# Kernel tuning notes

Hardware: AMD Instinct MI355X
Metric: run time of the kernel (lower is better)

## Reference

```python
import jax, jax.numpy as jnp
import numpy as np

E = 512        # embed_dim
H = 16         # num_heads
R = 8          # num_relation_heads
NH = H - R     # num_normal_heads
HD = E // H    # head_dim
SCALING = HD ** -0.5
B, LQ, LK = 2, 2048, 2048


def setup_inputs() -> dict:
    key = jax.random.key(0)
    ks = jax.random.split(key, 14)
    s = 1.0 / np.sqrt(E)  # keep pre-softmax logits moderate so exp() is stable
    inp = {
        "query": jax.random.normal(ks[0], (B, LQ, E), jnp.float32),
        "key": jax.random.normal(ks[1], (B, LK, E), jnp.float32),
        "value": jax.random.normal(ks[2], (B, LK, E), jnp.float32),
        "relation_weights": jax.random.uniform(ks[3], (B, R, LQ, LK), jnp.float32),
        "Wq": jax.random.normal(ks[4], (E, E), jnp.float32) * s,
        "bq": jnp.zeros((E,), jnp.float32),
        "Wk": jax.random.normal(ks[5], (E, E), jnp.float32) * s,
        "bk": jnp.zeros((E,), jnp.float32),
        "Wv": jax.random.normal(ks[6], (E, E), jnp.float32) * s,
        "bv": jnp.zeros((E,), jnp.float32),
        "Wo": jax.random.normal(ks[7], (E, E), jnp.float32) * s,
        "bo": jnp.zeros((E,), jnp.float32),
        "ln_gamma": jnp.ones((E,), jnp.float32),
        "ln_beta": jnp.zeros((E,), jnp.float32),
    }
    return inp


def reference(query, key, value, relation_weights, Wq, bq, Wk, bk, Wv, bv, Wo, bo, ln_gamma, ln_beta):
    b, lq, _ = query.shape
    lk = key.shape[1]
    # projections; weights stored as [in, out] so y = x @ W + b
    q = (query @ Wq + bq).reshape(b, lq, H, HD)
    k = (key @ Wk + bk).reshape(b, lk, H, HD)
    v = (value @ Wv + bv).reshape(b, lk, H, HD)
    # scores: [B, H, Lq, Lk]
    scores = jnp.einsum("bqhd,bkhd->bhqk", q, k) * SCALING
    # normal heads: standard softmax
    normal_attn = jax.nn.softmax(scores[:, :NH], axis=-1)
    # relation heads: exp(scores) * relation_weights, renormalized
    rel = jnp.exp(scores[:, NH:]) * relation_weights
    rel = rel / (rel.sum(axis=-1, keepdims=True) + 1e-6)
    attn = jnp.concatenate([normal_attn, rel], axis=1)  # [B, H, Lq, Lk]
    # weighted values -> [B, Lq, E]
    out = jnp.einsum("bhqk,bkhd->bqhd", attn, v).reshape(b, lq, E)
    out = out @ Wo + bo
    # LayerNorm (eps=1e-5, torch default)
    mu = out.mean(axis=-1, keepdims=True)
    var = out.var(axis=-1, keepdims=True)
    out = (out - mu) * jax.lax.rsqrt(var + 1e-5) * ln_gamma + ln_beta
    return out
```

## Files before the change

### kernel.cpp

```cpp
#include <hip/hip_runtime.h>


using u16 = unsigned short;
using u32 = unsigned int;

typedef __attribute__((ext_vector_type(8))) short bf16x8;
typedef __attribute__((ext_vector_type(4))) float f32x4;

#define H_  16
#define NH_ 8
#define HD_ 32
#define L_  2048
#define E_  512
#define B_  2
#define M_  4096
#define KSPLIT 2
static constexpr float SCALE_ = 0.1767766952966369f;

__device__ inline u16 f2bf(float x) {
  union { float f; u32 u; } v; v.f = x;
  u32 r = v.u + 0x7FFFu + ((v.u >> 16) & 1u);
  return (u16)(r >> 16);
}
__device__ inline u16 f2h(float x) {
  union { _Float16 h; u16 u; } v; v.h = (_Float16)x; return v.u;
}
__device__ inline float h2f(u16 x) {
  union { u16 u; _Float16 h; } v; v.u = x; return (float)v.h;
}

__global__ __launch_bounds__(256) void k_cvt3(const float* __restrict__ a, const float* __restrict__ b,
                                              const float* __restrict__ c,
                                              u16* __restrict__ oa, u16* __restrict__ ob, u16* __restrict__ oc) {
  int w = blockIdx.y;
  const float* s = (w == 0) ? a : (w == 1) ? b : c;
  u16* d = (w == 0) ? oa : (w == 1) ? ob : oc;
  size_t i = ((size_t)blockIdx.x * 256 + threadIdx.x) * 4;
  float4 v = *(const float4*)(s + i);
  uint2 pk;
  pk.x = (u32)f2bf(v.x) | ((u32)f2bf(v.y) << 16);
  pk.y = (u32)f2bf(v.z) | ((u32)f2bf(v.w) << 16);
  *(uint2*)(d + i) = pk;
}

__global__ __launch_bounds__(256) void k_wtrans(const float* __restrict__ Wq, const float* __restrict__ Wk,
                                                const float* __restrict__ Wv, const float* __restrict__ Wo,
                                                u16* __restrict__ Tq, u16* __restrict__ Tk,
                                                u16* __restrict__ Tv, u16* __restrict__ To) {
  int z = blockIdx.z;
  const float* W = (z == 0) ? Wq : (z == 1) ? Wk : (z == 2) ? Wv : Wo;
  u16* T = (z == 0) ? Tq : (z == 1) ? Tk : (z == 2) ? Tv : To;
  __shared__ u16 tile[64][65];
  int r0 = blockIdx.y * 64, c0 = blockIdx.x * 64;
  int tw = threadIdx.x >> 6, tl = threadIdx.x & 63;
#pragma unroll
  for (int i = 0; i < 16; ++i) {
    int r = i * 4 + tw;
    tile[r][tl] = f2bf(W[(size_t)(r0 + r) * E_ + c0 + tl]);
  }
  __syncthreads();
#pragma unroll
  for (int i = 0; i < 16; ++i) {
    int r = i * 4 + tw;
    T[(size_t)(c0 + r) * E_ + r0 + tl] = tile[tl][r];
  }
}

template <int MODE>
__device__ inline void gemm_body(const u16* __restrict__ A, const u16* __restrict__ Bt,
                                 const float* __restrict__ bias, void* __restrict__ out) {
  __shared__ __align__(16) u16 smem[2 * 128 * 72];
  u16* As = smem;
  u16* Bs = smem + 128 * 72;
  const int tid = threadIdx.x;
  const int lane = tid & 63, wid = tid >> 6;
  const int m0 = blockIdx.x * 128, n0 = blockIdx.y * 128;
  const int wm = (wid >> 1) * 64, wn = (wid & 1) * 64;
  const int mrow = lane & 15, quad = lane >> 4;
  f32x4 acc[4][4] = {};
  for (int k0 = 0; k0 < 512; k0 += 64) {
    __syncthreads();
#pragma unroll
    for (int i = 0; i < 4; ++i) {
      int task = i * 256 + tid;
      int r = task >> 3, c = task & 7;
      *(uint4*)(As + r * 72 + c * 8) = *(const uint4*)(A + (size_t)(m0 + r) * 512 + k0 + c * 8);
      *(uint4*)(Bs + r * 72 + c * 8) = *(const uint4*)(Bt + (size_t)(n0 + r) * 512 + k0 + c * 8);
    }
    __syncthreads();
#pragma unroll
    for (int kk = 0; kk < 64; kk += 32) {
      bf16x8 af[4], bfr[4];
#pragma unroll
      for (int f = 0; f < 4; ++f)
        af[f] = *(const bf16x8*)(As + (wm + f * 16 + mrow) * 72 + kk + quad * 8);
#pragma unroll
      for (int f = 0; f < 4; ++f)
        bfr[f] = *(const bf16x8*)(Bs + (wn + f * 16 + mrow) * 72 + kk + quad * 8);
#pragma unroll
      for (int fm = 0; fm < 4; ++fm)
#pragma unroll
        for (int fn = 0; fn < 4; ++fn)
          acc[fm][fn] = __builtin_amdgcn_mfma_f32_16x16x32_bf16(af[fm], bfr[fn], acc[fm][fn], 0, 0, 0);
    }
  }
  if (MODE == 0) {
    __syncthreads();
    u16* wscr = smem + wid * (64 * 72);
#pragma unroll
    for (int fn = 0; fn < 4; ++fn) {
      float bv = bias[n0 + wn + fn * 16 + mrow];
#pragma unroll
      for (int fm = 0; fm < 4; ++fm)
#pragma unroll
        for (int r = 0; r < 4; ++r)
          wscr[(fm * 16 + quad * 4 + r) * 72 + fn * 16 + mrow] = f2bf(acc[fm][fn][r] + bv);
    }
    asm volatile("s_waitcnt lgkmcnt(0)" ::: "memory");
    const int hg0 = (n0 + wn) >> 5;
#pragma unroll
    for (int c = 0; c < 8; ++c) {
      int linear = c * 64 + lane;
      int hh = linear >> 8;
      int rem = linear & 255;
      int lm = rem >> 2, j = rem & 3;
      uint4 vv = *(const uint4*)(wscr + lm * 72 + hh * 32 + j * 8);
      int gm = m0 + wm + lm;
      int bb = gm >> 11, q = gm & (L_ - 1);
      *(uint4*)((u16*)out + (((size_t)(bb * H_ + hg0 + hh)) * L_ + q) * HD_ + j * 8) = vv;
    }
  } else {
#pragma unroll
    for (int fn = 0; fn < 4; ++fn) {
      int gn = n0 + wn + fn * 16 + mrow;
      float bv = bias[gn];
#pragma unroll
      for (int fm = 0; fm < 4; ++fm)
#pragma unroll
        for (int r = 0; r < 4; ++r) {
          int gm = m0 + wm + fm * 16 + quad * 4 + r;
          ((float*)out)[(size_t)gm * E_ + gn] = acc[fm][fn][r] + bv;
        }
    }
  }
}

__global__ __launch_bounds__(256) void k_gemm_qkv(const u16* Xq, const u16* Xk, const u16* Xv,
                                                  const u16* Tq, const u16* Tk, const u16* Tv,
                                                  const float* bq, const float* bk, const float* bv,
                                                  u16* Qb, u16* Kb, u16* Vb) {
  int z = blockIdx.z;
  const u16* A = (z == 0) ? Xq : (z == 1) ? Xk : Xv;
  const u16* T = (z == 0) ? Tq : (z == 1) ? Tk : Tv;
  const float* bi = (z == 0) ? bq : (z == 1) ? bk : bv;
  u16* o = (z == 0) ? Qb : (z == 1) ? Kb : Vb;
  gemm_body<0>(A, T, bi, o);
}

__global__ __launch_bounds__(256) void k_gemm_o(const u16* A, const u16* T, const float* bi, float* Y) {
  gemm_body<1>(A, T, bi, Y);
}

__global__ __launch_bounds__(256) void k_vtrans(const u16* __restrict__ Vb, u16* __restrict__ Vt) {
  __shared__ u16 t[32 * 72];
  const int q0 = blockIdx.x * 64;
  const size_t headOff = (size_t)blockIdx.y * (L_ * HD_);
  const int tid = threadIdx.x;
  {
    int q = tid >> 2, c = tid & 3;
    uint4 v = *(const uint4*)(Vb + headOff + (size_t)(q0 + q) * HD_ + c * 8);
    const u16* s = (const u16*)&v;
#pragma unroll
    for (int i = 0; i < 8; ++i) t[(c * 8 + i) * 72 + q] = s[i];
  }
  __syncthreads();
  {
    int d = tid >> 3, j = tid & 7;
    uint4 o = *(const uint4*)(t + d * 72 + j * 8);
    *(uint4*)(Vt + headOff + (size_t)d * L_ + q0 + j * 8) = o;
  }
}

__global__ __launch_bounds__(256) void k_attn(const u16* __restrict__ Qb, const u16* __restrict__ Kb,
                                              const u16* __restrict__ Vt, const float* __restrict__ relw,
                                              u16* __restrict__ Pnum, float* __restrict__ Pden) {
  const int tid = threadIdx.x, lane = tid & 63, wid = tid >> 6;
  const int q0 = blockIdx.x * 64;
  const int h = blockIdx.y;
  const int b = blockIdx.z & (B_ - 1), s = blockIdx.z >> 1;
  const int kbase = s * (L_ / KSPLIT);
  const int kend = kbase + L_ / KSPLIT;
  const bool isrel = (h >= NH_);
  const size_t headOff = ((size_t)(b * H_ + h)) * L_ * HD_;
  const float* wbase = isrel ? relw + ((size_t)(b * (H_ - NH_) + (h - NH_))) * L_ * L_ : nullptr;

  __shared__ __align__(16) u16 Ps[4 * 16 * 68];
  u16* pw = Ps + wid * (16 * 68);

  const int mrow = lane & 15, quad = lane >> 4;
  const int qrow = q0 + wid * 16;
  bf16x8 qa = *(const bf16x8*)(Qb + headOff + (size_t)(qrow + mrow) * HD_ + quad * 8);
  f32x4 accd[2] = {};
  float den[4] = {0.f, 0.f, 0.f, 0.f};

  for (int kt = kbase; kt < kend; kt += 64) {
    bf16x8 kb[4];
#pragma unroll
    for (int f = 0; f < 4; ++f)
      kb[f] = *(const bf16x8*)(Kb + headOff + (size_t)(kt + f * 16 + mrow) * HD_ + quad * 8);
    bf16x8 vbf[2][2];
#pragma unroll
    for (int kk = 0; kk < 2; ++kk)
#pragma unroll
      for (int dh = 0; dh < 2; ++dh)
        vbf[kk][dh] = *(const bf16x8*)(Vt + headOff + (size_t)(dh * 16 + mrow) * L_ + kt + kk * 32 + quad * 8);
    float wv[4][4];
    if (isrel) {
#pragma unroll
      for (int f = 0; f < 4; ++f)
#pragma unroll
        for (int r = 0; r < 4; ++r)
          wv[f][r] = wbase[(size_t)(qrow + quad * 4 + r) * L_ + kt + f * 16 + mrow];
    }

    f32x4 sc[4];
#pragma unroll
    for (int f = 0; f < 4; ++f) {
      f32x4 z = {0.f, 0.f, 0.f, 0.f};
      sc[f] = __builtin_amdgcn_mfma_f32_16x16x32_bf16(qa, kb[f], z, 0, 0, 0);
    }
#pragma unroll
    for (int f = 0; f < 4; ++f)
#pragma unroll
      for (int r = 0; r < 4; ++r) {
        float e = __expf(sc[f][r] * SCALE_);
        if (isrel) e *= wv[f][r];
        den[r] += e;
        pw[(quad * 4 + r) * 68 + f * 16 + mrow] = f2bf(e);
      }
    asm volatile("s_waitcnt lgkmcnt(0)" ::: "memory");
#pragma unroll
    for (int kk = 0; kk < 2; ++kk) {
      bf16x8 pa = *(const bf16x8*)(pw + mrow * 68 + kk * 32 + quad * 8);
#pragma unroll
      for (int dh = 0; dh < 2; ++dh)
        accd[dh] = __builtin_amdgcn_mfma_f32_16x16x32_bf16(pa, vbf[kk][dh], accd[dh], 0, 0, 0);
    }
  }

#pragma unroll
  for (int off = 1; off < 16; off <<= 1)
#pragma unroll
    for (int r = 0; r < 4; ++r) den[r] += __shfl_xor(den[r], off, 64);

  const size_t pidx = ((size_t)(s * B_ + b) * H_ + h) * L_;
#pragma unroll
  for (int dh = 0; dh < 2; ++dh)
#pragma unroll
    for (int r = 0; r < 4; ++r) {
      int qg = qrow + quad * 4 + r;
      Pnum[(pidx + qg) * HD_ + dh * 16 + mrow] = f2h(accd[dh][r]);
    }
  if (mrow == 0) {
    int qg = qrow + quad * 4;
    float4 dv = {den[0], den[1], den[2], den[3]};
    *(float4*)(Pden + pidx + qg) = dv;
  }
}

__global__ __launch_bounds__(256) void k_combine(const u16* __restrict__ Pnum, const float* __restrict__ Pden,
                                                 u16* __restrict__ AO) {
  int row = blockIdx.x;
  int tid = threadIdx.x;
  int b = row >> 11, q = row & (L_ - 1);
  int e0 = tid * 2;
  int h = e0 >> 5, d = e0 & (HD_ - 1);
  size_t i0 = ((size_t)(0 * B_ + b) * H_ + h) * L_ + q;
  size_t i1 = ((size_t)(1 * B_ + b) * H_ + h) * L_ + q;
  u32 n0 = *(const u32*)(Pnum + i0 * HD_ + d);
  u32 n1 = *(const u32*)(Pnum + i1 * HD_ + d);
  float den = Pden[i0] + Pden[i1] + ((h >= NH_) ? 1e-6f : 0.f);
  float rinv = 1.0f / den;
  float x = (h2f((u16)n0) + h2f((u16)n1)) * rinv;
  float y = (h2f((u16)(n0 >> 16)) + h2f((u16)(n1 >> 16))) * rinv;
  u32 pk = (u32)f2bf(x) | ((u32)f2bf(y) << 16);
  *(u32*)(AO + (size_t)row * E_ + e0) = pk;
}

__global__ __launch_bounds__(256) void k_ln(const float* __restrict__ Y, const float* __restrict__ gamma,
                                            const float* __restrict__ beta, float* __restrict__ out) {
  int row = blockIdx.x, tid = threadIdx.x;
  const float* y = Y + (size_t)row * E_;
  float2 v = *(const float2*)(y + tid * 2);
  float s = v.x + v.y, sq = v.x * v.x + v.y * v.y;
#pragma unroll
  for (int off = 1; off < 64; off <<= 1) {
    s += __shfl_xor(s, off, 64);
    sq += __shfl_xor(sq, off, 64);
  }
  __shared__ float ss[4], ssq[4];
  int wid = tid >> 6, lane = tid & 63;
  if (lane == 0) { ss[wid] = s; ssq[wid] = sq; }
  __syncthreads();
  s = ss[0] + ss[1] + ss[2] + ss[3];
  sq = ssq[0] + ssq[1] + ssq[2] + ssq[3];
  float mean = s * (1.f / E_);
  float var = sq * (1.f / E_) - mean * mean;
  float rstd = rsqrtf(var + 1e-5f);
  float2 g = *(const float2*)(gamma + tid * 2);
  float2 be = *(const float2*)(beta + tid * 2);
  float2 o;
  o.x = (v.x - mean) * rstd * g.x + be.x;
  o.y = (v.y - mean) * rstd * g.y + be.y;
  *(float2*)(out + (size_t)row * E_ + tid * 2) = o;
}

extern "C" void kernel_launch(void* const* d_in, const int* in_sizes, int n_in,
                              void* d_out, int out_size, void* d_ws, size_t ws_size,
                              hipStream_t stream) {
  const float* query = (const float*)d_in[0];
  const float* key   = (const float*)d_in[1];
  const float* value = (const float*)d_in[2];
  const float* relw  = (const float*)d_in[3];
  const float* Wq = (const float*)d_in[4];
  const float* bq = (const float*)d_in[5];
  const float* Wk = (const float*)d_in[6];
  const float* bk = (const float*)d_in[7];
  const float* Wv = (const float*)d_in[8];
  const float* bv = (const float*)d_in[9];
  const float* Wo = (const float*)d_in[10];
  const float* bo = (const float*)d_in[11];
  const float* gamma = (const float*)d_in[12];
  const float* beta  = (const float*)d_in[13];

  char* ws = (char*)d_ws;
  u16* Xq = (u16*)(ws + 0);
  u16* Xk = (u16*)(ws + 4194304);
  u16* Xv = (u16*)(ws + 8388608);
  u16* Tq = (u16*)(ws + 12582912);
  u16* Tk = (u16*)(ws + 13107200);
  u16* Tv = (u16*)(ws + 13631488);
  u16* To = (u16*)(ws + 14155776);
  u16* Qb = (u16*)(ws + 14680064);
  u16* Kb = (u16*)(ws + 18874368);
  u16* Vb = (u16*)(ws + 23068672);
  u16* AO = (u16*)(ws + 27262976);
  u16* Vt = (u16*)(ws + 31457280);
  u16*   Pnum = (u16*)(ws + 0);
  float* Pden = (float*)(ws + 8388608);
  float* Y = (float*)(ws + 0);

  k_cvt3<<<dim3(2048, 3, 1), 256, 0, stream>>>(query, key, value, Xq, Xk, Xv);
  k_wtrans<<<dim3(8, 8, 4), 256, 0, stream>>>(Wq, Wk, Wv, Wo, Tq, Tk, Tv, To);
  k_gemm_qkv<<<dim3(32, 4, 3), 256, 0, stream>>>(Xq, Xk, Xv, Tq, Tk, Tv, bq, bk, bv, Qb, Kb, Vb);
  k_vtrans<<<dim3(32, 32, 1), 256, 0, stream>>>(Vb, Vt);
  k_attn<<<dim3(32, 16, B_ * KSPLIT), 256, 0, stream>>>(Qb, Kb, Vt, relw, Pnum, Pden);
  k_combine<<<M_, 256, 0, stream>>>(Pnum, Pden, AO);
  k_gemm_o<<<dim3(32, 4, 1), 256, 0, stream>>>(AO, To, bo, Y);
  k_ln<<<M_, 256, 0, stream>>>(Y, gamma, beta, (float*)d_out);
}
```

Baseline: 513.5 us.

## Split attention into templated normal/relation kernels and raise key split to four

```diff
diff --git a/kernel.cpp b/kernel.cpp
--- a/kernel.cpp
+++ b/kernel.cpp
@@ -14,7 +14,7 @@
 #define E_  512
 #define B_  2
 #define M_  4096
-#define KSPLIT 2
+#define KS  4
 static constexpr float SCALE_ = 0.1767766952966369f;
 
 __device__ inline u16 f2bf(float x) {
@@ -181,18 +181,18 @@
   }
 }
 
-__global__ __launch_bounds__(256) void k_attn(const u16* __restrict__ Qb, const u16* __restrict__ Kb,
-                                              const u16* __restrict__ Vt, const float* __restrict__ relw,
-                                              u16* __restrict__ Pnum, float* __restrict__ Pden) {
+template <int ISREL>
+__global__ __launch_bounds__(256) void k_attn_t(const u16* __restrict__ Qb, const u16* __restrict__ Kb,
+                                                const u16* __restrict__ Vt, const float* __restrict__ relw,
+                                                u16* __restrict__ Pnum, float* __restrict__ Pden) {
   const int tid = threadIdx.x, lane = tid & 63, wid = tid >> 6;
   const int q0 = blockIdx.x * 64;
-  const int h = blockIdx.y;
+  const int h = blockIdx.y + (ISREL ? NH_ : 0);
   const int b = blockIdx.z & (B_ - 1), s = blockIdx.z >> 1;
-  const int kbase = s * (L_ / KSPLIT);
-  const int kend = kbase + L_ / KSPLIT;
-  const bool isrel = (h >= NH_);
+  const int kbase = s * (L_ / KS);
+  const int kend = kbase + L_ / KS;
   const size_t headOff = ((size_t)(b * H_ + h)) * L_ * HD_;
-  const float* wbase = isrel ? relw + ((size_t)(b * (H_ - NH_) + (h - NH_))) * L_ * L_ : nullptr;
+  const float* wbase = ISREL ? relw + ((size_t)(b * (H_ - NH_) + blockIdx.y)) * L_ * L_ : nullptr;
 
   __shared__ __align__(16) u16 Ps[4 * 16 * 68];
   u16* pw = Ps + wid * (16 * 68);
@@ -215,7 +215,7 @@
       for (int dh = 0; dh < 2; ++dh)
         vbf[kk][dh] = *(const bf16x8*)(Vt + headOff + (size_t)(dh * 16 + mrow) * L_ + kt + kk * 32 + quad * 8);
     float wv[4][4];
-    if (isrel) {
+    if (ISREL) {
 #pragma unroll
       for (int f = 0; f < 4; ++f)
 #pragma unroll
@@ -234,7 +234,7 @@
 #pragma unroll
       for (int r = 0; r < 4; ++r) {
         float e = __expf(sc[f][r] * SCALE_);
-        if (isrel) e *= wv[f][r];
+        if (ISREL) e *= wv[f][r];
         den[r] += e;
         pw[(quad * 4 + r) * 68 + f * 16 + mrow] = f2bf(e);
       }
@@ -275,15 +275,17 @@
   int b = row >> 11, q = row & (L_ - 1);
   int e0 = tid * 2;
   int h = e0 >> 5, d = e0 & (HD_ - 1);
-  size_t i0 = ((size_t)(0 * B_ + b) * H_ + h) * L_ + q;
-  size_t i1 = ((size_t)(1 * B_ + b) * H_ + h) * L_ + q;
-  u32 n0 = *(const u32*)(Pnum + i0 * HD_ + d);
-  u32 n1 = *(const u32*)(Pnum + i1 * HD_ + d);
-  float den = Pden[i0] + Pden[i1] + ((h >= NH_) ? 1e-6f : 0.f);
+  float x = 0.f, y = 0.f, den = (h >= NH_) ? 1e-6f : 0.f;
+#pragma unroll
+  for (int s = 0; s < KS; ++s) {
+    size_t is = ((size_t)(s * B_ + b) * H_ + h) * L_ + q;
+    u32 n = *(const u32*)(Pnum + is * HD_ + d);
+    x += h2f((u16)n);
+    y += h2f((u16)(n >> 16));
+    den += Pden[is];
+  }
   float rinv = 1.0f / den;
-  float x = (h2f((u16)n0) + h2f((u16)n1)) * rinv;
-  float y = (h2f((u16)(n0 >> 16)) + h2f((u16)(n1 >> 16))) * rinv;
-  u32 pk = (u32)f2bf(x) | ((u32)f2bf(y) << 16);
+  u32 pk = (u32)f2bf(x * rinv) | ((u32)f2bf(y * rinv) << 16);
   *(u32*)(AO + (size_t)row * E_ + e0) = pk;
 }
 
@@ -346,15 +348,16 @@
   u16* Vb = (u16*)(ws + 23068672);
   u16* AO = (u16*)(ws + 27262976);
   u16* Vt = (u16*)(ws + 31457280);
-  u16*   Pnum = (u16*)(ws + 0);
-  float* Pden = (float*)(ws + 8388608);
+  u16*   Pnum = (u16*)(ws + 35651584);
+  float* Pden = (float*)(ws + 52428800);
   float* Y = (float*)(ws + 0);
 
   k_cvt3<<<dim3(2048, 3, 1), 256, 0, stream>>>(query, key, value, Xq, Xk, Xv);
   k_wtrans<<<dim3(8, 8, 4), 256, 0, stream>>>(Wq, Wk, Wv, Wo, Tq, Tk, Tv, To);
   k_gemm_qkv<<<dim3(32, 4, 3), 256, 0, stream>>>(Xq, Xk, Xv, Tq, Tk, Tv, bq, bk, bv, Qb, Kb, Vb);
   k_vtrans<<<dim3(32, 32, 1), 256, 0, stream>>>(Vb, Vt);
-  k_attn<<<dim3(32, 16, B_ * KSPLIT), 256, 0, stream>>>(Qb, Kb, Vt, relw, Pnum, Pden);
+  k_attn_t<0><<<dim3(32, NH_, B_ * KS), 256, 0, stream>>>(Qb, Kb, Vt, relw, Pnum, Pden);
+  k_attn_t<1><<<dim3(32, H_ - NH_, B_ * KS), 256, 0, stream>>>(Qb, Kb, Vt, relw, Pnum, Pden);
   k_combine<<<M_, 256, 0, stream>>>(Pnum, Pden, AO);
   k_gemm_o<<<dim3(32, 4, 1), 256, 0, stream>>>(AO, To, bo, Y);
   k_ln<<<M_, 256, 0, stream>>>(Y, gamma, beta, (float*)d_out);
```

Result: slower. 531.4 us (+3.5%).
